# Performance work log

Measured on AMD Instinct MI355X. Metric: run time of the kernel, lower is better.

## Reference

```python
import jax, jax.numpy as jnp
import numpy as np

PATCH = 16


def setup_inputs() -> dict:
    key = jax.random.key(0)
    x = jax.random.normal(key, (256, 3, 224, 224), dtype=jnp.float32)
    return {"x": x}


def reference(x):
    P = PATCH
    B, C, Hi, Wi = x.shape
    h, w = Hi // P, Wi // P  # grid rows (h) and cols (w)
    # 'b c (h p1) (w p2) -> b w h p1 p2 c'
    patches = x.reshape(B, C, h, P, w, P).transpose(0, 4, 2, 3, 5, 1)  # (B, w, h, p1, p2, C)
    # center_rotate: transpose p1<->p2 for patches with grid col j in [w/3, 2w/3]
    # and grid row k in [h/3, 2h/3] (original skips j < W/3 or j > 2W/3, same for k)
    jw = jnp.arange(w)
    kh = jnp.arange(h)
    mw = (jw >= w / 3) & (jw <= 2 * w / 3)
    mh = (kh >= h / 3) & (kh <= 2 * h / 3)
    mask = (mw[:, None] & mh[None, :])[None, :, :, None, None, None]  # (1, w, h, 1, 1, 1)
    rot = jnp.where(mask, jnp.swapaxes(patches, 3, 4), patches)  # (B, w, h, a3, a4, C)
    # 'b w h p2 p1 c -> b c (h p2) (w p1)': axis3 is read as p2 (inner height),
    # axis4 as p1 (inner width) -- i.e. every patch gets transposed on reassembly,
    # so center patches (transposed twice) come back in original orientation.
    out = rot.transpose(0, 5, 2, 3, 1, 4).reshape(B, C, h * P, w * P)
    return out
```

## Files before the change

kernel.cpp:

```cpp
#include <hip/hip_runtime.h>


#define W4 56
#define IMG_F4 12544
#define NIDENT_BLKS 37632

typedef float vf4 __attribute__((ext_vector_type(4)));

__global__ __launch_bounds__(256) void patch_rotate_kernel(
    const float* __restrict__ x, float* __restrict__ out) {
  const int tid = threadIdx.x;

  if (blockIdx.x < NIDENT_BLKS) {
    const int idx = blockIdx.x * 256 + tid;
    const int rem = idx % IMG_F4;
    const int row = rem / W4;
    const int col4 = rem % W4;
    const int k = row >> 4;
    const int j = col4 >> 2;
    const bool center = (j >= 5) & (j <= 9) & (k >= 5) & (k <= 9);
    if (!center) {
      vf4 v = __builtin_nontemporal_load((const vf4*)x + idx);
      __builtin_nontemporal_store(v, (vf4*)out + idx);
    }
    return;
  }

  __shared__ float ldsT[4][16][20];
  const int pb = blockIdx.x - NIDENT_BLKS;
  const int lp = tid >> 6;
  const int l  = tid & 63;
  const int p  = pb * 4 + lp;
  const int q  = p / 25;
  const int pi = p % 25;
  const int kk = 5 + pi / 5;
  const int jj = 5 + pi % 5;
  const float* __restrict__ xs = x + (size_t)q * (IMG_F4 * 4);
  float* __restrict__ os = out + (size_t)q * (IMG_F4 * 4);

  const int r  = l >> 2;
  const int c0 = (l & 3) << 2;

  const vf4 v = __builtin_nontemporal_load(
      (const vf4*)(xs + (kk * 16 + r) * 224 + jj * 16 + c0));
  ldsT[lp][c0 + 0][r] = v.x;
  ldsT[lp][c0 + 1][r] = v.y;
  ldsT[lp][c0 + 2][r] = v.z;
  ldsT[lp][c0 + 3][r] = v.w;

  __syncthreads();

  vf4 w;
  w.x = ldsT[lp][r][c0 + 0];
  w.y = ldsT[lp][r][c0 + 1];
  w.z = ldsT[lp][r][c0 + 2];
  w.w = ldsT[lp][r][c0 + 3];
  __builtin_nontemporal_store(
      w, (vf4*)(os + (kk * 16 + r) * 224 + jj * 16 + c0));
}

extern "C" void kernel_launch(void* const* d_in, const int* in_sizes, int n_in,
                              void* d_out, int out_size, void* d_ws, size_t ws_size,
                              hipStream_t stream) {
  const float* x = (const float*)d_in[0];
  float* out = (float*)d_out;
  const int blocks = NIDENT_BLKS + 4800;
  patch_rotate_kernel<<<blocks, 256, 0, stream>>>(x, out);
}
```

Baseline: 251.8 us.

## Replace identity-copy blocks with hipMemcpyAsync plus small center-patch fixup kernel

The custom identity-copy path is replaced by a full device-to-device hipMemcpyAsync of the whole tensor. A second kernel with only the center-patch blocks then overwrites the 25 center patches per channel image with their transposed contents. The aim is to use the runtime's tuned copy (possibly the SDMA engine) for the bulk traffic. In exchange the center region is written twice, and there is an extra launch plus a serial dependency between the copy and the fixup kernel.

```diff
diff --git a/kernel.cpp b/kernel.cpp
--- a/kernel.cpp
+++ b/kernel.cpp
@@ -1,42 +1,23 @@
 #include <hip/hip_runtime.h>
 
 
-#define W4 56
-#define IMG_F4 12544
-#define NIDENT_BLKS 37632
+#define IMG_F 50176
+#define TOTAL_BYTES ((size_t)256 * 3 * 224 * 224 * 4)
 
 typedef float vf4 __attribute__((ext_vector_type(4)));
 
-__global__ __launch_bounds__(256) void patch_rotate_kernel(
+__global__ __launch_bounds__(256) void center_fixup(
     const float* __restrict__ x, float* __restrict__ out) {
-  const int tid = threadIdx.x;
-
-  if (blockIdx.x < NIDENT_BLKS) {
-    const int idx = blockIdx.x * 256 + tid;
-    const int rem = idx % IMG_F4;
-    const int row = rem / W4;
-    const int col4 = rem % W4;
-    const int k = row >> 4;
-    const int j = col4 >> 2;
-    const bool center = (j >= 5) & (j <= 9) & (k >= 5) & (k <= 9);
-    if (!center) {
-      vf4 v = __builtin_nontemporal_load((const vf4*)x + idx);
-      __builtin_nontemporal_store(v, (vf4*)out + idx);
-    }
-    return;
-  }
-
   __shared__ float ldsT[4][16][20];
-  const int pb = blockIdx.x - NIDENT_BLKS;
-  const int lp = tid >> 6;
-  const int l  = tid & 63;
-  const int p  = pb * 4 + lp;
+  const int lp = threadIdx.x >> 6;
+  const int l  = threadIdx.x & 63;
+  const int p  = blockIdx.x * 4 + lp;
   const int q  = p / 25;
   const int pi = p % 25;
   const int kk = 5 + pi / 5;
   const int jj = 5 + pi % 5;
-  const float* __restrict__ xs = x + (size_t)q * (IMG_F4 * 4);
-  float* __restrict__ os = out + (size_t)q * (IMG_F4 * 4);
+  const float* __restrict__ xs = x + (size_t)q * IMG_F;
+  float* __restrict__ os = out + (size_t)q * IMG_F;
 
   const int r  = l >> 2;
   const int c0 = (l & 3) << 2;
@@ -64,6 +45,6 @@
                               hipStream_t stream) {
   const float* x = (const float*)d_in[0];
   float* out = (float*)d_out;
-  const int blocks = NIDENT_BLKS + 4800;
-  patch_rotate_kernel<<<blocks, 256, 0, stream>>>(x, out);
+  hipMemcpyAsync(out, x, TOTAL_BYTES, hipMemcpyDeviceToDevice, stream);
+  center_fixup<<<4800, 256, 0, stream>>>(x, out);
 }
```

After: 269.7 us. 1.07x slower.
